# Optimization experiments

Hardware: AMD Instinct MI355X
Metric: run time of the kernel (lower is better)

## Reference

```python
import jax, jax.numpy as jnp
import numpy as np

B, S, D, H = 2, 2048, 1024, 16
DK = D // H

def setup_inputs() -> dict:
    key = jax.random.key(0)
    ks = jax.random.split(key, 11)
    s = 1.0 / np.sqrt(D)
    inp = {
        'q': jax.random.normal(ks[0], (B, S, D), jnp.float32),
        'k': jax.random.normal(ks[1], (B, S, D), jnp.float32),
        'v': jax.random.normal(ks[2], (B, S, D), jnp.float32),
        'mask': jnp.tril(jnp.ones((S, S), jnp.bool_))[None, None],  # [1,1,S,S] causal
        'w_q': jax.random.normal(ks[3], (D, D), jnp.float32) * s,
        'b_q': jax.random.normal(ks[4], (D,), jnp.float32) * s,
        'w_k': jax.random.normal(ks[5], (D, D), jnp.float32) * s,
        'b_k': jax.random.normal(ks[6], (D,), jnp.float32) * s,
        'w_v': jax.random.normal(ks[7], (D, D), jnp.float32) * s,
        'b_v': jax.random.normal(ks[8], (D,), jnp.float32) * s,
        'w_o': jax.random.normal(ks[9], (D, D), jnp.float32) * s,
        'b_o': jax.random.normal(ks[10], (D,), jnp.float32) * s,
    }
    return inp

def reference(q, k, v, mask, w_q, b_q, w_k, b_k, w_v, b_v, w_o, b_o):
    # Linear projections (torch Linear: x @ W^T + b)
    qh = (q @ w_q.T + b_q).reshape(B, S, H, DK).transpose(0, 2, 1, 3)  # [B,H,S,DK]
    kh = (k @ w_k.T + b_k).reshape(B, S, H, DK).transpose(0, 2, 1, 3)
    vh = (v @ w_v.T + b_v).reshape(B, S, H, DK).transpose(0, 2, 1, 3)
    scores = jnp.einsum('bhqd,bhkd->bhqk', qh, kh) / jnp.sqrt(jnp.float32(DK))
    scores = jnp.where(mask, scores, jnp.float32(-jnp.inf))
    attn = jax.nn.softmax(scores, axis=-1)  # dropout p=0.0 -> identity
    out = jnp.einsum('bhqk,bhkd->bhqd', attn, vh)
    out = out.transpose(0, 2, 1, 3).reshape(B, S, D)
    return out @ w_o.T + b_o
```

## Files before the change

kernel.cpp:

```cpp
#include <hip/hip_runtime.h>
#include <hip/hip_bf16.h>

typedef __bf16 bf16_t;
typedef __bf16 bf16x4 __attribute__((ext_vector_type(4)));
typedef __bf16 bf16x8 __attribute__((ext_vector_type(8)));
typedef float f32x4 __attribute__((ext_vector_type(4)));

#define B_ 2
#define S_ 2048
#define D_ 1024
#define H_ 16
#define DK_ 64
#define M_ (B_ * S_)

__device__ __forceinline__ f32x4 mfma16(bf16x8 a, bf16x8 b, f32x4 c) {
  return __builtin_amdgcn_mfma_f32_16x16x32_bf16(a, b, c, 0, 0, 0);
}

__device__ __forceinline__ void async_load16(const bf16_t* g, bf16_t* l) {
  __builtin_amdgcn_global_load_lds(
      (const __attribute__((address_space(1))) void*)g,
      (__attribute__((address_space(3))) void*)l, 16, 0, 0);
}


__global__ void cvt_all(const float* __restrict__ q, const float* __restrict__ k,
                        const float* __restrict__ v, const float* __restrict__ w0,
                        const float* __restrict__ w1, const float* __restrict__ w2,
                        const float* __restrict__ w3, bf16_t* __restrict__ qb,
                        bf16_t* __restrict__ kb, bf16_t* __restrict__ vb,
                        bf16_t* __restrict__ o0, bf16_t* __restrict__ o1,
                        bf16_t* __restrict__ o2, bf16_t* __restrict__ o3) {
  const int y = blockIdx.y;
  if (y >= 3 && blockIdx.x >= 512) return;
  const float* src;
  bf16_t* dst;
  float sc = 1.0f;
  switch (y) {
    case 0: src = q; dst = qb; break;
    case 1: src = k; dst = kb; break;
    case 2: src = v; dst = vb; break;
    case 3: src = w0; dst = o0; sc = 0.125f; break;
    case 4: src = w1; dst = o1; break;
    case 5: src = w2; dst = o2; break;
    default: src = w3; dst = o3; break;
  }
  long i = ((long)blockIdx.x * blockDim.x + threadIdx.x) * 8;
  const float4* s4 = (const float4*)(src + i);
  float4 a = s4[0], b = s4[1];
  bf16x8 o;
  o[0] = (bf16_t)(a.x * sc); o[1] = (bf16_t)(a.y * sc);
  o[2] = (bf16_t)(a.z * sc); o[3] = (bf16_t)(a.w * sc);
  o[4] = (bf16_t)(b.x * sc); o[5] = (bf16_t)(b.y * sc);
  o[6] = (bf16_t)(b.z * sc); o[7] = (bf16_t)(b.w * sc);
  *(bf16x8*)(dst + i) = o;
}


__device__ __forceinline__ int swzG(int b) {
  return b ^ (((b >> 7) & 7) << 4);
}

template <int NR>
__device__ __forceinline__ void stage_tile(const bf16_t* g, bf16_t* lds,
                                           const int* srcoff, int wave) {
#pragma unroll
  for (int rnd = 0; rnd < NR; ++rnd)
    async_load16(g + srcoff[rnd], lds + rnd * 2048 + wave * 512);
}

template <int MODE>
__device__ __forceinline__ void gemm_core(const bf16_t* __restrict__ A,
                                          const bf16_t* __restrict__ W,
                                          const float* __restrict__ bias,
                                          float bscale, void* __restrict__ Cv,
                                          bf16_t* __restrict__ As,
                                          bf16_t* __restrict__ Bs) {
  constexpr int N = 1024, K = 1024;
  constexpr int TILE = 128 * 32;
  const int tid = threadIdx.x;
  const int wave = tid >> 6, lane = tid & 63;
  const int quad = lane >> 4, l15 = lane & 15;
  const int wm = wave >> 1, wn = wave & 1;
  const int bm = blockIdx.x * 128, bn = blockIdx.y * 128;

  f32x4 acc[4][4] = {};

  int srcoff[2];
#pragma unroll
  for (int rnd = 0; rnd < 2; ++rnd) {
    const int bb = rnd * 4096 + tid * 16;
    const int sb = swzG(bb);
    srcoff[rnd] = (sb >> 6) * K + ((sb & 63) >> 1);
  }
  const bf16_t* ag = A + (long)bm * K;
  const bf16_t* bg = W + (long)bn * K;

  const int xorv = ((l15 >> 1) & 7) << 4;
  const int aco = (((wm * 64 + l15) * 64 + quad * 16) ^ xorv) >> 1;
  const int bco = (((wn * 64 + l15) * 64 + quad * 16) ^ xorv) >> 1;

  stage_tile<2>(ag, As, srcoff, wave);
  stage_tile<2>(bg, Bs, srcoff, wave);

  int cur = 0;
  for (int kk = 0; kk < K; kk += 32) {
    if (kk + 32 < K) {
      stage_tile<2>(ag + kk + 32, As + (cur ^ 1) * TILE, srcoff, wave);
      stage_tile<2>(bg + kk + 32, Bs + (cur ^ 1) * TILE, srcoff, wave);
      asm volatile("s_waitcnt vmcnt(4)" ::: "memory");
    } else {
      asm volatile("s_waitcnt vmcnt(0)" ::: "memory");
    }
    __builtin_amdgcn_sched_barrier(0);
    __builtin_amdgcn_s_barrier();
    __builtin_amdgcn_sched_barrier(0);

    const bf16_t* Ac = As + cur * TILE;
    const bf16_t* Bc = Bs + cur * TILE;
    bf16x8 af[4], bfr[4];
#pragma unroll
    for (int i = 0; i < 4; ++i)
      af[i] = *(const bf16x8*)&Ac[aco + i * 512];
#pragma unroll
    for (int i = 0; i < 4; ++i)
      bfr[i] = *(const bf16x8*)&Bc[bco + i * 512];
    __builtin_amdgcn_s_setprio(1);
#pragma unroll
    for (int mi = 0; mi < 4; ++mi)
#pragma unroll
      for (int ni = 0; ni < 4; ++ni)
        acc[mi][ni] = mfma16(af[mi], bfr[ni], acc[mi][ni]);
    __builtin_amdgcn_s_setprio(0);

    asm volatile("s_waitcnt lgkmcnt(0)" ::: "memory");
    __builtin_amdgcn_sched_barrier(0);
    __builtin_amdgcn_s_barrier();
    __builtin_amdgcn_sched_barrier(0);
    cur ^= 1;
  }

#pragma unroll
  for (int mi = 0; mi < 4; ++mi) {
#pragma unroll
    for (int ni = 0; ni < 4; ++ni) {
      const int col = bn + wn * 64 + ni * 16 + l15;
      const float bsv = bias[col] * bscale;
      f32x4 v = acc[mi][ni];
      const int row0 = bm + wm * 64 + mi * 16 + quad * 4;
      if (MODE == 3) {
        float* C = (float*)Cv;
#pragma unroll
        for (int r = 0; r < 4; ++r)
          C[(long)(row0 + r) * N + col] = v[r] + bsv;
      } else if (MODE == 1) {
        bf16_t* C = (bf16_t*)Cv;
        const int hh = col >> 6, dk = col & 63;
        const int bq = row0 >> 11, s0 = row0 & 2047;
        bf16_t* base = C + (((long)bq * H_ + hh) * S_ + s0) * DK_ + dk;
#pragma unroll
        for (int r = 0; r < 4; ++r)
          base[(long)r * DK_] = (bf16_t)(v[r] + bsv);
      } else {
        bf16_t* C = (bf16_t*)Cv;
        const int hh = col >> 6, dk = col & 63;
        const int bq = row0 >> 11, s0 = row0 & 2047;
        bf16x4 pk;
#pragma unroll
        for (int r = 0; r < 4; ++r) pk[r] = (bf16_t)(v[r] + bsv);
        *(bf16x4*)(C + (((long)bq * H_ + hh) * DK_ + dk) * S_ + s0) = pk;
      }
    }
  }
}

__global__ __launch_bounds__(256) void gemm_qkv(
    const bf16_t* __restrict__ qb, const bf16_t* __restrict__ kb,
    const bf16_t* __restrict__ vb, const bf16_t* __restrict__ wq,
    const bf16_t* __restrict__ wk, const bf16_t* __restrict__ wv,
    const float* __restrict__ biq, const float* __restrict__ bik,
    const float* __restrict__ biv, bf16_t* __restrict__ Qh,
    bf16_t* __restrict__ Kh, bf16_t* __restrict__ Vt) {
  __shared__ bf16_t As[2][128 * 32];
  __shared__ bf16_t Bs[2][128 * 32];
  if (blockIdx.z == 0)
    gemm_core<1>(qb, wq, biq, 0.125f, Qh, &As[0][0], &Bs[0][0]);
  else if (blockIdx.z == 1)
    gemm_core<1>(kb, wk, bik, 1.0f, Kh, &As[0][0], &Bs[0][0]);
  else
    gemm_core<2>(vb, wv, biv, 1.0f, Vt, &As[0][0], &Bs[0][0]);
}

__device__ __forceinline__ int swzG128(int b) {
  return b ^ (((b >> 7) & 7) << 4);
}

template <int NR>
__device__ __forceinline__ void stage_tile128(const bf16_t* g, bf16_t* lds,
                                              const int* srcoff, int wave) {
#pragma unroll
  for (int rnd = 0; rnd < NR; ++rnd)
    async_load16(g + srcoff[rnd], lds + rnd * 2048 + wave * 512);
}

__global__ __launch_bounds__(256) void gemm_out64(
    const bf16_t* __restrict__ AO, const bf16_t* __restrict__ wo,
    const float* __restrict__ bo, float* __restrict__ out) {
  constexpr int N = 1024, K = 1024;
  __shared__ bf16_t As[2][64 * 64];
  __shared__ bf16_t Bs[2][128 * 64];
  const int tid = threadIdx.x;
  const int wave = tid >> 6, lane = tid & 63;
  const int quad = lane >> 4, l15 = lane & 15;
  const int wm = wave >> 1, wn = wave & 1;
  const int bm = blockIdx.x * 64, bn = blockIdx.y * 128;

  f32x4 acc[2][4] = {};

  int srcoff[4];
#pragma unroll
  for (int rnd = 0; rnd < 4; ++rnd) {
    const int bb = rnd * 4096 + tid * 16;
    const int sb = swzG128(bb);
    srcoff[rnd] = (sb >> 7) * K + ((sb & 127) >> 1);
  }
  const bf16_t* ag = AO + (long)bm * K;
  const bf16_t* bg = wo + (long)bn * K;

  const int co0 = ((quad * 16) ^ ((l15 & 7) << 4)) >> 1;
  const int co1 = ((quad * 16 + 64) ^ ((l15 & 7) << 4)) >> 1;
  const int arow0 = (wm * 32 + l15) * 64;
  const int brow0 = (wn * 64 + l15) * 64;

  stage_tile128<2>(ag, &As[0][0], srcoff, wave);
  stage_tile128<4>(bg, &Bs[0][0], srcoff, wave);

  int cur = 0;
  for (int kk = 0; kk < K; kk += 64) {
    if (kk + 64 < K) {
      stage_tile128<2>(ag + kk + 64, &As[cur ^ 1][0], srcoff, wave);
      stage_tile128<4>(bg + kk + 64, &Bs[cur ^ 1][0], srcoff, wave);
      asm volatile("s_waitcnt vmcnt(6)" ::: "memory");
    } else {
      asm volatile("s_waitcnt vmcnt(0)" ::: "memory");
    }
    __builtin_amdgcn_sched_barrier(0);
    __builtin_amdgcn_s_barrier();
    __builtin_amdgcn_sched_barrier(0);

#pragma unroll
    for (int h = 0; h < 2; ++h) {
      const int co = h ? co1 : co0;
      bf16x8 af[2], bfr[4];
#pragma unroll
      for (int i = 0; i < 2; ++i)
        af[i] = *(const bf16x8*)&As[cur][arow0 + i * 1024 + co];
#pragma unroll
      for (int i = 0; i < 4; ++i)
        bfr[i] = *(const bf16x8*)&Bs[cur][brow0 + i * 1024 + co];
      __builtin_amdgcn_s_setprio(1);
#pragma unroll
      for (int mi = 0; mi < 2; ++mi)
#pragma unroll
        for (int ni = 0; ni < 4; ++ni)
          acc[mi][ni] = mfma16(af[mi], bfr[ni], acc[mi][ni]);
      __builtin_amdgcn_s_setprio(0);
    }

    asm volatile("s_waitcnt lgkmcnt(0)" ::: "memory");
    __builtin_amdgcn_sched_barrier(0);
    __builtin_amdgcn_s_barrier();
    __builtin_amdgcn_sched_barrier(0);
    cur ^= 1;
  }

#pragma unroll
  for (int mi = 0; mi < 2; ++mi) {
#pragma unroll
    for (int ni = 0; ni < 4; ++ni) {
      const int col = bn + wn * 64 + ni * 16 + l15;
      const float bsv = bo[col];
      f32x4 v = acc[mi][ni];
      const int row0 = bm + wm * 32 + mi * 16 + quad * 4;
#pragma unroll
      for (int r = 0; r < 4; ++r)
        out[(long)(row0 + r) * N + col] = v[r] + bsv;
    }
  }
}


__device__ __forceinline__ int swzK(int b) {
  return b ^ (((b >> 7) & 3) << 4) ^ (((b >> 10) & 1) << 6);
}
__device__ __forceinline__ int swzV(int b) {
  return b ^ (((b >> 7) & 7) << 4);
}

template <bool MASKED>
__device__ __forceinline__ void softmax_pa(const f32x4 st[4], float& l_i,
                                           bf16x8& pa0, bf16x8& pa1,
                                           const int qcol, const int quad) {
#pragma unroll
  for (int nb = 0; nb < 4; ++nb) {
    const int kvb = quad * 8 + (nb & 1) * 4 + (nb >> 1) * 32;
#pragma unroll
    for (int r = 0; r < 4; ++r) {
      float x = st[nb][r];
      if (MASKED && (kvb + r) > qcol) x = -30000.f;
      const float pv = __expf(x);
      l_i += pv;
      const bf16_t pb = (bf16_t)pv;
      const int idx = ((nb & 1) << 2) | r;
      if (nb < 2) pa0[idx] = pb;
      else        pa1[idx] = pb;
    }
  }
}

__global__ __launch_bounds__(256, 3) void flash_attn3(
    const bf16_t* __restrict__ Qh, const bf16_t* __restrict__ Kh,
    const bf16_t* __restrict__ Vt, bf16_t* __restrict__ Po,
    float* __restrict__ Pl) {
  const int bid = blockIdx.x;
  const int g = bid & 31;
  const int z = bid >> 5;
  const int i = z / 3, pi = z % 3;
  const int h = g & 15, b = g >> 4;
  const int tA = i, tB = 31 - i;
  const int tid = threadIdx.x, wave = tid >> 6, lane = tid & 63;
  const int quad = lane >> 4, l15 = lane & 15;
  const int qcol = wave * 16 + l15;
  const int prow = ((l15 >> 2) << 3) | (l15 & 3);

  __shared__ bf16_t Kls[2][64 * 64];
  __shared__ bf16_t Vls[2][64 * 64];

  const bf16_t* qhead = Qh + ((long)(b * H_ + h) * S_) * DK_;
  const bf16_t* khead = Kh + ((long)(b * H_ + h) * S_) * DK_;
  const bf16_t* vhead = Vt + ((long)(b * H_ + h) * DK_) * S_;

  int koffe[2], voffe[2], ldse[2];
#pragma unroll
  for (int c = 0; c < 2; ++c) {
    const int bb = c * 4096 + wave * 1024 + lane * 16;
    koffe[c] = swzK(bb) >> 1;
    const int vs = swzV(bb);
    voffe[c] = (vs >> 7) * S_ + ((vs & 127) >> 1);
    ldse[c] = c * 2048 + wave * 512;
  }

  int kro[4][2], vro[4][2];
#pragma unroll
  for (int nb = 0; nb < 4; ++nb) {
    const int krow = prow + (nb & 1) * 4 + (nb >> 1) * 32;
    const int vrow = nb * 16 + l15;
#pragma unroll
    for (int hh = 0; hh < 2; ++hh) {
      kro[nb][hh] = swzK(krow * 128 + quad * 16 + hh * 64) >> 1;
      vro[nb][hh] = swzV(vrow * 128 + quad * 16 + hh * 64) >> 1;
    }
  }

  const int qA = tA * 64 + wave * 16;
  const int qB = tB * 64 + wave * 16;
  const bf16_t* qpA = qhead + (long)(qA + l15) * DK_ + quad * 8;
  const bf16_t* qpB = qhead + (long)(qB + l15) * DK_ + quad * 8;
  const bf16x8 aqA0 = *(const bf16x8*)qpA;
  const bf16x8 aqA1 = *(const bf16x8*)(qpA + 32);
  const bf16x8 aqB0 = *(const bf16x8*)qpB;
  const bf16x8 aqB1 = *(const bf16x8*)(qpB + 32);

  f32x4 oA[4] = {}, oB[4] = {};
  float lA = 0.f, lB = 0.f;

  {
    const bf16_t* kt = khead + pi * (64 * DK_);
    const bf16_t* vt = vhead + pi * 64;
#pragma unroll
    for (int c = 0; c < 2; ++c) {
      async_load16(kt + koffe[c], &Kls[0][ldse[c]]);
      async_load16(vt + voffe[c], &Vls[0][ldse[c]]);
    }
  }

  int cur = 0;
  for (int j = pi; j <= tB; j += 3) {
    const bool pf = (j + 3 <= tB);
    if (pf) {
      const bf16_t* kt = khead + (j + 3) * (64 * DK_);
      const bf16_t* vt = vhead + (j + 3) * 64;
#pragma unroll
      for (int c = 0; c < 2; ++c) {
        async_load16(kt + koffe[c], &Kls[cur ^ 1][ldse[c]]);
        async_load16(vt + voffe[c], &Vls[cur ^ 1][ldse[c]]);
      }
      asm volatile("s_waitcnt vmcnt(4)" ::: "memory");
    } else {
      asm volatile("s_waitcnt vmcnt(0)" ::: "memory");
    }
    __builtin_amdgcn_sched_barrier(0);
    __builtin_amdgcn_s_barrier();
    __builtin_amdgcn_sched_barrier(0);

    const bf16_t* Kc = &Kls[cur][0];
    const bf16_t* Vc = &Vls[cur][0];

    bf16x8 k0[4], k1[4];
#pragma unroll
    for (int nb = 0; nb < 4; ++nb) {
      k0[nb] = *(const bf16x8*)&Kc[kro[nb][0]];
      k1[nb] = *(const bf16x8*)&Kc[kro[nb][1]];
    }

    bf16x8 paB0, paB1, paA0, paA1;
    {
      f32x4 stB[4];
#pragma unroll
      for (int nb = 0; nb < 4; ++nb) {
        f32x4 t = {};
        t = mfma16(k0[nb], aqB0, t);
        t = mfma16(k1[nb], aqB1, t);
        stB[nb] = t;
      }
      if (j == tB)
        softmax_pa<true>(stB, lB, paB0, paB1, qcol, quad);
      else
        softmax_pa<false>(stB, lB, paB0, paB1, qcol, quad);
    }
    const bool doA = (j <= tA);
    if (doA) {
      f32x4 stA[4];
#pragma unroll
      for (int nb = 0; nb < 4; ++nb) {
        f32x4 t = {};
        t = mfma16(k0[nb], aqA0, t);
        t = mfma16(k1[nb], aqA1, t);
        stA[nb] = t;
      }
      if (j == tA)
        softmax_pa<true>(stA, lA, paA0, paA1, qcol, quad);
      else
        softmax_pa<false>(stA, lA, paA0, paA1, qcol, quad);
    }

    bf16x8 v0[4], v1[4];
#pragma unroll
    for (int nb = 0; nb < 4; ++nb) {
      v0[nb] = *(const bf16x8*)&Vc[vro[nb][0]];
      v1[nb] = *(const bf16x8*)&Vc[vro[nb][1]];
    }
#pragma unroll
    for (int nb = 0; nb < 4; ++nb) {
      oB[nb] = mfma16(paB0, v0[nb], oB[nb]);
      oB[nb] = mfma16(paB1, v1[nb], oB[nb]);
    }
    if (doA) {
#pragma unroll
      for (int nb = 0; nb < 4; ++nb) {
        oA[nb] = mfma16(paA0, v0[nb], oA[nb]);
        oA[nb] = mfma16(paA1, v1[nb], oA[nb]);
      }
    }

    asm volatile("s_waitcnt lgkmcnt(0)" ::: "memory");
    __builtin_amdgcn_sched_barrier(0);
    __builtin_amdgcn_s_barrier();
    __builtin_amdgcn_sched_barrier(0);
    cur ^= 1;
  }

  lA += __shfl_xor(lA, 16, 64);
  lA += __shfl_xor(lA, 32, 64);
  lB += __shfl_xor(lB, 16, 64);
  lB += __shfl_xor(lB, 32, 64);

  bf16_t* po = Po + (long)pi * (M_ * D_);
  bf16_t* poA = po + (long)(b * S_ + qA + quad * 4) * D_ + h * DK_ + l15;
  bf16_t* poB = po + (long)(b * S_ + qB + quad * 4) * D_ + h * DK_ + l15;
#pragma unroll
  for (int r = 0; r < 4; ++r) {
#pragma unroll
    for (int nb = 0; nb < 4; ++nb) {
      poA[(long)r * D_ + nb * 16] = (bf16_t)oA[nb][r];
      poB[(long)r * D_ + nb * 16] = (bf16_t)oB[nb][r];
    }
  }

  if (quad == 0) {
    float* pl = Pl + (long)pi * (B_ * H_ * S_) + (long)(b * H_ + h) * S_;
    pl[qA + l15] = lA;
    pl[qB + l15] = lB;
  }
}


__global__ __launch_bounds__(256) void merge_po(const bf16_t* __restrict__ Po,
                                                const float* __restrict__ Pl,
                                                bf16_t* __restrict__ AO) {
  const long e = ((long)blockIdx.x * 256 + threadIdx.x) * 8;
  const int bs = (int)(e >> 10);
  const int d = (int)(e & 1023);
  const int h = d >> 6;
  const int b = bs >> 11, s = bs & 2047;
  const long lidx = ((long)(b * H_ + h)) * S_ + s;

  float acc[8] = {0.f, 0.f, 0.f, 0.f, 0.f, 0.f, 0.f, 0.f};
  float L = 0.f;
#pragma unroll
  for (int p = 0; p < 3; ++p) {
    bf16x8 x = *(const bf16x8*)(Po + (long)p * (M_ * D_) + e);
#pragma unroll
    for (int k = 0; k < 8; ++k) acc[k] += (float)x[k];
    L += Pl[(long)p * (B_ * H_ * S_) + lidx];
  }
  const float inv = 1.f / L;
  bf16x8 y;
#pragma unroll
  for (int k = 0; k < 8; ++k) y[k] = (bf16_t)(acc[k] * inv);
  *(bf16x8*)(AO + e) = y;
}


extern "C" void kernel_launch(void* const* d_in, const int* in_sizes, int n_in,
                              void* d_out, int out_size, void* d_ws, size_t ws_size,
                              hipStream_t stream) {
  const float* q = (const float*)d_in[0];
  const float* k = (const float*)d_in[1];
  const float* v = (const float*)d_in[2];
  const float* wq = (const float*)d_in[4];
  const float* bq = (const float*)d_in[5];
  const float* wk = (const float*)d_in[6];
  const float* bk = (const float*)d_in[7];
  const float* wv = (const float*)d_in[8];
  const float* bv = (const float*)d_in[9];
  const float* wo = (const float*)d_in[10];
  const float* bo = (const float*)d_in[11];
  float* out = (float*)d_out;

  char* ws = (char*)d_ws;
  const size_t MB = 1024 * 1024;
  bf16_t* Qh = (bf16_t*)(ws);
  bf16_t* Kh = (bf16_t*)(ws + 8 * MB);
  bf16_t* Vt = (bf16_t*)(ws + 16 * MB);
  bf16_t* AO = (bf16_t*)(ws + 24 * MB);
  bf16_t* qb = (bf16_t*)(ws + 32 * MB);
  bf16_t* kb = (bf16_t*)(ws + 40 * MB);
  bf16_t* vb = (bf16_t*)(ws + 48 * MB);
  bf16_t* wqb = (bf16_t*)(ws + 56 * MB);
  bf16_t* wkb = (bf16_t*)(ws + 58 * MB);
  bf16_t* wvb = (bf16_t*)(ws + 60 * MB);
  bf16_t* wob = (bf16_t*)(ws + 62 * MB);
  bf16_t* Po = (bf16_t*)(ws + 32 * MB);
  float* Pl = (float*)(ws + 56 * MB);

  cvt_all<<<dim3(2048, 7, 1), 256, 0, stream>>>(q, k, v, wq, wk, wv, wo, qb, kb,
                                                vb, wqb, wkb, wvb, wob);
  gemm_qkv<<<dim3(32, 8, 3), 256, 0, stream>>>(qb, kb, vb, wqb, wkb, wvb, bq, bk,
                                               bv, Qh, Kh, Vt);
  flash_attn3<<<dim3(1536, 1, 1), 256, 0, stream>>>(Qh, Kh, Vt, Po, Pl);
  merge_po<<<dim3(2048, 1, 1), 256, 0, stream>>>(Po, Pl, AO);
  gemm_out64<<<dim3(64, 8, 1), 256, 0, stream>>>(AO, wob, bo, out);
}
```

Measured before the change: 214.5 us.

## Triple-buffer LDS in QKV and output GEMMs with one barrier per iteration

Both projection GEMMs move from double to triple LDS buffering and prefetch two k-tiles ahead. The trailing lgkmcnt wait and second barrier of each iteration are removed. Issuing the next load after the single barrier is safe because the buffer it overwrites was last read two iterations earlier. This cuts barrier stalls per k-step and deepens global-to-LDS overlap, at the cost of 1.5x the LDS footprint, which could lower occupancy.

Measured after the change: 216.9 us. About the same (+1.1%).

```diff
diff --git a/kernel.cpp b/kernel.cpp
--- a/kernel.cpp
+++ b/kernel.cpp
@@ -78,6 +78,7 @@
                                           bf16_t* __restrict__ Bs) {
   constexpr int N = 1024, K = 1024;
   constexpr int TILE = 128 * 32;
+  constexpr int NIT = K / 32;
   const int tid = threadIdx.x;
   const int wave = tid >> 6, lane = tid & 63;
   const int quad = lane >> 4, l15 = lane & 15;
@@ -102,22 +103,29 @@
 
   stage_tile<2>(ag, As, srcoff, wave);
   stage_tile<2>(bg, Bs, srcoff, wave);
-
-  int cur = 0;
-  for (int kk = 0; kk < K; kk += 32) {
-    if (kk + 32 < K) {
-      stage_tile<2>(ag + kk + 32, As + (cur ^ 1) * TILE, srcoff, wave);
-      stage_tile<2>(bg + kk + 32, Bs + (cur ^ 1) * TILE, srcoff, wave);
+  stage_tile<2>(ag + 32, As + TILE, srcoff, wave);
+  stage_tile<2>(bg + 32, Bs + TILE, srcoff, wave);
+
+  int rb = 0, sb2 = 2;
+  for (int j = 0; j < NIT; ++j) {
+    if (j < NIT - 1)
       asm volatile("s_waitcnt vmcnt(4)" ::: "memory");
-    } else {
+    else
       asm volatile("s_waitcnt vmcnt(0)" ::: "memory");
-    }
     __builtin_amdgcn_sched_barrier(0);
     __builtin_amdgcn_s_barrier();
     __builtin_amdgcn_sched_barrier(0);
 
-    const bf16_t* Ac = As + cur * TILE;
-    const bf16_t* Bc = Bs + cur * TILE;
+    if (j + 2 < NIT) {
+      const int kk2 = (j + 2) * 32;
+      stage_tile<2>(ag + kk2, As + sb2 * TILE, srcoff, wave);
+      stage_tile<2>(bg + kk2, Bs + sb2 * TILE, srcoff, wave);
+    }
+    sb2 = (sb2 == 2) ? 0 : sb2 + 1;
+
+    const bf16_t* Ac = As + rb * TILE;
+    const bf16_t* Bc = Bs + rb * TILE;
+    rb = (rb == 2) ? 0 : rb + 1;
     bf16x8 af[4], bfr[4];
 #pragma unroll
     for (int i = 0; i < 4; ++i)
@@ -132,12 +140,6 @@
       for (int ni = 0; ni < 4; ++ni)
         acc[mi][ni] = mfma16(af[mi], bfr[ni], acc[mi][ni]);
     __builtin_amdgcn_s_setprio(0);
-
-    asm volatile("s_waitcnt lgkmcnt(0)" ::: "memory");
-    __builtin_amdgcn_sched_barrier(0);
-    __builtin_amdgcn_s_barrier();
-    __builtin_amdgcn_sched_barrier(0);
-    cur ^= 1;
   }
 
 #pragma unroll
@@ -181,8 +183,8 @@
     const float* __restrict__ biq, const float* __restrict__ bik,
     const float* __restrict__ biv, bf16_t* __restrict__ Qh,
     bf16_t* __restrict__ Kh, bf16_t* __restrict__ Vt) {
-  __shared__ bf16_t As[2][128 * 32];
-  __shared__ bf16_t Bs[2][128 * 32];
+  __shared__ bf16_t As[3][128 * 32];
+  __shared__ bf16_t Bs[3][128 * 32];
   if (blockIdx.z == 0)
     gemm_core<1>(qb, wq, biq, 0.125f, Qh, &As[0][0], &Bs[0][0]);
   else if (blockIdx.z == 1)
@@ -195,20 +197,14 @@
   return b ^ (((b >> 7) & 7) << 4);
 }
 
-template <int NR>
-__device__ __forceinline__ void stage_tile128(const bf16_t* g, bf16_t* lds,
-                                              const int* srcoff, int wave) {
-#pragma unroll
-  for (int rnd = 0; rnd < NR; ++rnd)
-    async_load16(g + srcoff[rnd], lds + rnd * 2048 + wave * 512);
-}
-
 __global__ __launch_bounds__(256) void gemm_out64(
     const bf16_t* __restrict__ AO, const bf16_t* __restrict__ wo,
     const float* __restrict__ bo, float* __restrict__ out) {
   constexpr int N = 1024, K = 1024;
-  __shared__ bf16_t As[2][64 * 64];
-  __shared__ bf16_t Bs[2][128 * 64];
+  constexpr int ATILE = 64 * 64, BTILE = 128 * 64;
+  constexpr int NIT = K / 64;
+  __shared__ bf16_t As[3][ATILE];
+  __shared__ bf16_t Bs[3][BTILE];
   const int tid = threadIdx.x;
   const int wave = tid >> 6, lane = tid & 63;
   const int quad = lane >> 4, l15 = lane & 15;
@@ -232,32 +228,41 @@
   const int arow0 = (wm * 32 + l15) * 64;
   const int brow0 = (wn * 64 + l15) * 64;
 
-  stage_tile128<2>(ag, &As[0][0], srcoff, wave);
-  stage_tile128<4>(bg, &Bs[0][0], srcoff, wave);
-
-  int cur = 0;
-  for (int kk = 0; kk < K; kk += 64) {
-    if (kk + 64 < K) {
-      stage_tile128<2>(ag + kk + 64, &As[cur ^ 1][0], srcoff, wave);
-      stage_tile128<4>(bg + kk + 64, &Bs[cur ^ 1][0], srcoff, wave);
+  stage_tile<2>(ag, &As[0][0], srcoff, wave);
+  stage_tile<4>(bg, &Bs[0][0], srcoff, wave);
+  stage_tile<2>(ag + 64, &As[1][0], srcoff, wave);
+  stage_tile<4>(bg + 64, &Bs[1][0], srcoff, wave);
+
+  int rb = 0, sb2 = 2;
+  for (int j = 0; j < NIT; ++j) {
+    if (j < NIT - 1)
       asm volatile("s_waitcnt vmcnt(6)" ::: "memory");
-    } else {
+    else
       asm volatile("s_waitcnt vmcnt(0)" ::: "memory");
-    }
     __builtin_amdgcn_sched_barrier(0);
     __builtin_amdgcn_s_barrier();
     __builtin_amdgcn_sched_barrier(0);
 
+    if (j + 2 < NIT) {
+      const int kk2 = (j + 2) * 64;
+      stage_tile<2>(ag + kk2, &As[sb2][0], srcoff, wave);
+      stage_tile<4>(bg + kk2, &Bs[sb2][0], srcoff, wave);
+    }
+    sb2 = (sb2 == 2) ? 0 : sb2 + 1;
+
+    const bf16_t* Ac = &As[rb][0];
+    const bf16_t* Bc = &Bs[rb][0];
+    rb = (rb == 2) ? 0 : rb + 1;
 #pragma unroll
     for (int h = 0; h < 2; ++h) {
       const int co = h ? co1 : co0;
       bf16x8 af[2], bfr[4];
 #pragma unroll
       for (int i = 0; i < 2; ++i)
-        af[i] = *(const bf16x8*)&As[cur][arow0 + i * 1024 + co];
+        af[i] = *(const bf16x8*)&Ac[arow0 + i * 1024 + co];
 #pragma unroll
       for (int i = 0; i < 4; ++i)
-        bfr[i] = *(const bf16x8*)&Bs[cur][brow0 + i * 1024 + co];
+        bfr[i] = *(const bf16x8*)&Bc[brow0 + i * 1024 + co];
       __builtin_amdgcn_s_setprio(1);
 #pragma unroll
       for (int mi = 0; mi < 2; ++mi)
@@ -266,12 +271,6 @@
           acc[mi][ni] = mfma16(af[mi], bfr[ni], acc[mi][ni]);
       __builtin_amdgcn_s_setprio(0);
     }
-
-    asm volatile("s_waitcnt lgkmcnt(0)" ::: "memory");
-    __builtin_amdgcn_sched_barrier(0);
-    __builtin_amdgcn_s_barrier();
-    __builtin_amdgcn_sched_barrier(0);
-    cur ^= 1;
   }
 
 #pragma unroll
```
